# Performance work log

Hardware: AMD Instinct MI355X
Metric: run time of the kernel (lower is better)

## Reference

```python
import jax, jax.numpy as jnp
import numpy as np

D = 512      # d_model
S = 8        # num_quantum_states
B, T = 16, 1024
LN_EPS = 1e-5


def setup_inputs() -> dict:
    key = jax.random.key(0)
    ks = jax.random.split(key, 10)
    sc = lambda fan_in: 1.0 / np.sqrt(fan_in)
    return {
        "x": jax.random.normal(ks[0], (B, T, D), dtype=jnp.float32),
        # entanglement gates: torch Linear weight [out=D, in=2D], bias [D], stacked over S
        "W_ent": jax.random.uniform(ks[1], (S, D, 2 * D), minval=-sc(2 * D), maxval=sc(2 * D)),
        "b_ent": jax.random.uniform(ks[2], (S, D), minval=-sc(2 * D), maxval=sc(2 * D)),
        # measurement MLP: Linear(D*S->D), LayerNorm(D), Tanh, Linear(D->1)
        "m1_w": jax.random.uniform(ks[3], (D, D * S), minval=-sc(D * S), maxval=sc(D * S)),
        "m1_b": jax.random.uniform(ks[4], (D,), minval=-sc(D * S), maxval=sc(D * S)),
        "ln_g": jnp.ones((D,), dtype=jnp.float32),
        "ln_b": jnp.zeros((D,), dtype=jnp.float32),
        "m2_w": jax.random.uniform(ks[5], (1, D), minval=-sc(D), maxval=sc(D)),
        "m2_b": jax.random.uniform(ks[6], (1,), minval=-sc(D), maxval=sc(D)),
    }


def _layernorm(h, g, b):
    mu = jnp.mean(h, axis=-1, keepdims=True)
    var = jnp.mean(jnp.square(h - mu), axis=-1, keepdims=True)
    return (h - mu) * jax.lax.rsqrt(var + LN_EPS) * g + b


def reference(x, W_ent, b_ent, m1_w, m1_b, ln_g, ln_b, m2_w, m2_b):
    b_, t_, d_ = x.shape
    s_ = W_ent.shape[0]
    # gate(cat[x_i, x_j]).mean(dim=2) == x_i @ W1^T + mean_j(x_j) @ W2^T + b  (exact algebra)
    W1 = W_ent[:, :, :d_]   # [S, D, D] acts on x_i
    W2 = W_ent[:, :, d_:]   # [S, D, D] acts on x_j (mean over j)
    xbar = jnp.mean(x, axis=1)                                   # [B, D]
    ent = (jnp.einsum('btd,sed->bste', x, W1)                    # [B, S, T, D]
           + jnp.einsum('bd,sed->bse', xbar, W2)[:, :, None, :]
           + b_ent[None, :, None, :])
    # permute(0,2,3,1).reshape(B,T,D*S): feature layout is (d, s) fastest on s
    qv = jnp.transpose(ent, (0, 2, 3, 1)).reshape(b_, t_, d_ * s_)
    h = jnp.tanh(_layernorm(qv @ m1_w.T + m1_b, ln_g, ln_b))     # [B, T, D]
    attn_logits = h @ m2_w.T + m2_b                              # [B, T, 1]
    attn_weights = jax.nn.softmax(attn_logits, axis=1)
    context = jnp.sum(attn_weights * x, axis=1)                  # [B, D]
    return context, attn_weights
```

## Files before the change

kernel.cpp:

```cpp
#include <hip/hip_runtime.h>
#include <hip/hip_bf16.h>

typedef __attribute__((ext_vector_type(8))) short bf16x8;
typedef __attribute__((ext_vector_type(4))) float f32x4;

__device__ __forceinline__ float bf2f(unsigned short u) {
    union { unsigned int i; float f; } c; c.i = ((unsigned int)u) << 16; return c.f;
}
__device__ __forceinline__ unsigned short f2bf(float f) {
    union { float f; unsigned int i; } c; c.f = f;
    unsigned int x = c.i;
    x += 0x7fffu + ((x >> 16) & 1u);
    return (unsigned short)(x >> 16);
}
__device__ __forceinline__ unsigned int pk2(float a, float b) {
    __hip_bfloat162 h = __float22bfloat162_rn(float2{a, b});
    union { __hip_bfloat162 h; unsigned int u; } c; c.h = h; return c.u;
}
__device__ __forceinline__ float tanh_fast(float v) {
    float a = fabsf(v);
    a = fminf(a, 15.0f);
    float e = __expf(2.0f * a);
    float t = 1.0f - 2.0f / (e + 1.0f);
    return copysignf(t, v);
}

#define GLOAD_LDS16(gp, lp) \
    __builtin_amdgcn_global_load_lds((const __attribute__((address_space(1))) void*)(gp), \
                                     (__attribute__((address_space(3))) void*)(lp), 16, 0, 0)

#define MFMA(a, b, c) __builtin_amdgcn_mfma_f32_16x16x32_bf16((a), (b), (c), 0, 0, 0)

#define SBAR()  __builtin_amdgcn_s_barrier()
#define SCHED0() __builtin_amdgcn_sched_barrier(0)


__global__ void k_sumx(const float* __restrict__ x, float* __restrict__ sumx) {
    int b = blockIdx.x, tc = blockIdx.y;
    int tid = threadIdx.x;
    const float* xp = x + ((size_t)b * 1024 + tc * 64) * 512;
    float a0 = 0.f, a1 = 0.f;
    for (int t = 0; t < 64; ++t) {
        a0 += xp[(size_t)t * 512 + tid];
        a1 += xp[(size_t)t * 512 + tid + 256];
    }
    atomicAdd(&sumx[b * 512 + tid], a0);
    atomicAdd(&sumx[b * 512 + tid + 256], a1);
}

__global__ void k_prepA(const float* __restrict__ m1w, const float* __restrict__ bent,
                        unsigned short* __restrict__ Abf, float* __restrict__ bias2) {
    int i = blockIdx.x, tid = threadIdx.x;
    const float* row = m1w + (size_t)i * 4096;
    float acc = 0.f;
    #pragma unroll
    for (int q = 0; q < 4; ++q) {
        int col = q * 1024 + tid * 4;
        float4 v = *(const float4*)(row + col);
        ushort4 o;
        o.x = f2bf(v.x); o.y = f2bf(v.y); o.z = f2bf(v.z); o.w = f2bf(v.w);
        *(ushort4*)(Abf + (size_t)i * 4096 + col) = o;
        int e0 = col >> 3, s0 = col & 7;
        acc += v.x * bent[(s0    ) * 512 + e0];
        acc += v.y * bent[(s0 + 1) * 512 + e0];
        acc += v.z * bent[(s0 + 2) * 512 + e0];
        acc += v.w * bent[(s0 + 3) * 512 + e0];
    }
    #pragma unroll
    for (int off = 32; off; off >>= 1) acc += __shfl_xor(acc, off);
    __shared__ float r4[4];
    if ((tid & 63) == 0) r4[tid >> 6] = acc;
    __syncthreads();
    if (tid == 0) bias2[i] = r4[0] + r4[1] + r4[2] + r4[3];
}

__global__ void k_conv_W(const float* __restrict__ W, unsigned short* __restrict__ WT) {
    __shared__ float tile[128][33];
    int e0 = blockIdx.x * 16;
    int j0 = blockIdx.y * 32;
    int tid = threadIdx.x;
    int tx = tid & 31, ty = tid >> 5;
    #pragma unroll
    for (int q = 0; q < 16; ++q) {
        int lk = q * 8 + ty;
        int de = lk >> 3, s = lk & 7;
        int r = s * 512 + e0 + de;
        tile[lk][tx] = W[(size_t)r * 1024 + j0 + tx];
    }
    __syncthreads();
    int j = tid >> 3, ck = (tid & 7) * 16;
    unsigned short* dst = WT + (size_t)(j0 + j) * 4096 + e0 * 8 + ck;
    #pragma unroll
    for (int g = 0; g < 4; ++g) {
        ushort4 o;
        o.x = f2bf(tile[ck + g * 4 + 0][j]);
        o.y = f2bf(tile[ck + g * 4 + 1][j]);
        o.z = f2bf(tile[ck + g * 4 + 2][j]);
        o.w = f2bf(tile[ck + g * 4 + 3][j]);
        *(ushort4*)(dst + g * 4) = o;
    }
}

__launch_bounds__(512, 2)
__global__ void k_gemm1(const unsigned short* __restrict__ Abf,
                        const unsigned short* __restrict__ WT,
                        float* __restrict__ CpL, float* __restrict__ CpR) {
    __shared__ __align__(16) unsigned short sA[2][64 * 64];
    __shared__ __align__(16) unsigned short sB[2][256 * 64];
    int i0 = blockIdx.x * 64;
    int j0 = blockIdx.y * 256;
    int kbase = blockIdx.z * 512;
    int tid = threadIdx.x, lane = tid & 63, w = tid >> 6;
    int wm = w >> 2, wn = w & 3;
    int lr = lane >> 3, sl = lane & 7;
    int lo = lane & 15, hi = lane >> 4;
    int arow = w * 8 + lr;
    const unsigned short* gA = Abf + (size_t)(i0 + arow) * 4096 + kbase + ((sl ^ lr) << 3);
    const unsigned short* gB0 = WT + (size_t)(j0 + w * 32 + 0 * 8 + lr) * 4096 + kbase + ((sl ^ lr) << 3);
    const unsigned short* gB1 = WT + (size_t)(j0 + w * 32 + 1 * 8 + lr) * 4096 + kbase + ((sl ^ lr) << 3);
    const unsigned short* gB2 = WT + (size_t)(j0 + w * 32 + 2 * 8 + lr) * 4096 + kbase + ((sl ^ lr) << 3);
    const unsigned short* gB3 = WT + (size_t)(j0 + w * 32 + 3 * 8 + lr) * 4096 + kbase + ((sl ^ lr) << 3);
    bool left = (blockIdx.y < 2);
    f32x4 acc[2][4] = {};

#define G1_STAGE(tt, bufn)                                                    \
    do {                                                                      \
        int koff = (tt) * 64;                                                 \
        GLOAD_LDS16(gA + koff, &sA[bufn][w * 8 * 64]);                        \
        GLOAD_LDS16(gB0 + koff, &sB[bufn][(w * 32 + 0) * 64]);                \
        GLOAD_LDS16(gB1 + koff, &sB[bufn][(w * 32 + 8) * 64]);                \
        GLOAD_LDS16(gB2 + koff, &sB[bufn][(w * 32 + 16) * 64]);               \
        GLOAD_LDS16(gB3 + koff, &sB[bufn][(w * 32 + 24) * 64]);               \
        SCHED0();                                                             \
    } while (0)

    G1_STAGE(0, 0);
    #pragma unroll
    for (int t = 0; t < 8; ++t) {
        int buf = t & 1;
        if (t < 7) {
            G1_STAGE(t + 1, buf ^ 1);
            asm volatile("s_waitcnt vmcnt(5)" ::: "memory");
        } else {
            asm volatile("s_waitcnt vmcnt(0)" ::: "memory");
        }
        SCHED0(); SBAR(); SCHED0();
        __builtin_amdgcn_s_setprio(1);
        #pragma unroll
        for (int kk = 0; kk < 2; ++kk) {
            int slotX = ((kk * 4 + hi) ^ (lo & 7)) << 3;
            bf16x8 a0 = *(const bf16x8*)(&sA[buf][(wm * 32 +      lo) * 64 + slotX]);
            bf16x8 a1 = *(const bf16x8*)(&sA[buf][(wm * 32 + 16 + lo) * 64 + slotX]);
            #pragma unroll
            for (int n = 0; n < 4; ++n) {
                bf16x8 bb = *(const bf16x8*)(&sB[buf][(wn * 64 + n * 16 + lo) * 64 + slotX]);
                if (left) {
                    acc[0][n] = MFMA(a0, bb, acc[0][n]);
                    acc[1][n] = MFMA(a1, bb, acc[1][n]);
                } else {
                    acc[0][n] = MFMA(bb, a0, acc[0][n]);
                    acc[1][n] = MFMA(bb, a1, acc[1][n]);
                }
            }
        }
        __builtin_amdgcn_s_setprio(0);
        if (t < 7) { SCHED0(); SBAR(); SCHED0(); }
    }
#undef G1_STAGE

    int ksoff = blockIdx.z * 262144;
    if (left) {
        #pragma unroll
        for (int m = 0; m < 2; ++m) {
            int ib = i0 + wm * 32 + m * 16 + hi * 4;
            #pragma unroll
            for (int n = 0; n < 4; ++n) {
                int j = j0 + wn * 64 + n * 16 + lo;
                #pragma unroll
                for (int r = 0; r < 4; ++r)
                    CpL[ksoff + (ib + r) * 512 + j] = acc[m][n][r];
            }
        }
    } else {
        #pragma unroll
        for (int m = 0; m < 2; ++m) {
            int ic = i0 + wm * 32 + m * 16 + lo;
            #pragma unroll
            for (int n = 0; n < 4; ++n) {
                int db = j0 - 512 + wn * 64 + n * 16 + hi * 4;
                #pragma unroll
                for (int r = 0; r < 4; ++r)
                    CpR[ksoff + (db + r) * 512 + ic] = acc[m][n][r];
            }
        }
    }
}

__global__ void k_reduce(const float* __restrict__ CpL, const float* __restrict__ CpR,
                         unsigned short* __restrict__ M1bf, unsigned short* __restrict__ M2t) {
    int bx = blockIdx.x;
    const float* Cp = (bx < 256) ? CpL : CpR;
    unsigned short* ob = (bx < 256) ? M1bf : M2t;
    int gid = (bx & 255) * 256 + threadIdx.x;
    float4 s = ((const float4*)Cp)[gid];
    #pragma unroll
    for (int ks = 1; ks < 8; ++ks) {
        float4 t = ((const float4*)Cp)[ks * 65536 + gid];
        s.x += t.x; s.y += t.y; s.z += t.z; s.w += t.w;
    }
    ushort4 o;
    o.x = f2bf(s.x); o.y = f2bf(s.y); o.z = f2bf(s.z); o.w = f2bf(s.w);
    ((ushort4*)ob)[gid] = o;
}

__global__ void k_cb(const float* __restrict__ sumx, const unsigned short* __restrict__ M2t,
                     const float* __restrict__ bias2, const float* __restrict__ m1b,
                     float* __restrict__ cbo) {
    int b = blockIdx.x, i0 = blockIdx.y * 64;
    int tid = threadIdx.x;
    int il = tid & 63, dq = tid >> 6;
    const float* sx = sumx + b * 512 + dq * 128;
    const unsigned short* mp = M2t + (size_t)dq * 128 * 512 + i0 + il;
    float acc = 0.f;
    #pragma unroll 4
    for (int dd = 0; dd < 128; ++dd)
        acc += sx[dd] * bf2f(mp[(size_t)dd * 512]);
    __shared__ float sPart[4][64];
    sPart[dq][il] = acc;
    __syncthreads();
    if (tid < 64) {
        float v = sPart[0][tid] + sPart[1][tid] + sPart[2][tid] + sPart[3][tid];
        cbo[b * 512 + i0 + tid] = v * (1.0f / 1024.0f) + bias2[i0 + tid] + m1b[i0 + tid];
    }
}

__launch_bounds__(512)
__global__ void k_gemm2s(const float* __restrict__ x,
                         const unsigned short* __restrict__ M1bf,
                         unsigned short* __restrict__ ypk) {
    __shared__ __align__(16) unsigned short sA[64 * 64];
    __shared__ __align__(16) unsigned short sB[512 * 64];
    int bt0 = blockIdx.x * 64;
    int tid = threadIdx.x, lane = tid & 63, w = tid >> 6;
    int wm = w >> 2, wn = w & 3;
    int lo = lane & 15, hi = lane >> 4;
    int lr = lane >> 3, sl = lane & 7;
    int arow = tid >> 3, aslot = tid & 7;
    const float* gA = x + (size_t)(bt0 + arow) * 512 + aslot * 8;
    unsigned short* dAp = sA + arow * 64 + ((aslot ^ (arow & 7)) << 3);
    const unsigned short* gB[8];
    #pragma unroll
    for (int g = 0; g < 8; ++g)
        gB[g] = M1bf + (size_t)(w * 64 + g * 8 + lr) * 512 + ((sl ^ lr) << 3);
    f32x4 acc[2][8] = {};
    for (int k0 = 0; k0 < 512; k0 += 64) {
        if (k0) __syncthreads();
        #pragma unroll
        for (int g = 0; g < 8; ++g)
            GLOAD_LDS16(gB[g] + k0, &sB[(w * 64 + g * 8) * 64]);
        float4 f0 = *(const float4*)(gA + k0);
        float4 f1 = *(const float4*)(gA + k0 + 4);
        bf16x8 pk;
        pk[0] = (short)f2bf(f0.x); pk[1] = (short)f2bf(f0.y);
        pk[2] = (short)f2bf(f0.z); pk[3] = (short)f2bf(f0.w);
        pk[4] = (short)f2bf(f1.x); pk[5] = (short)f2bf(f1.y);
        pk[6] = (short)f2bf(f1.z); pk[7] = (short)f2bf(f1.w);
        *(bf16x8*)dAp = pk;
        __syncthreads();
        #pragma unroll
        for (int kk = 0; kk < 2; ++kk) {
            int slotX = ((kk * 4 + hi) ^ (lo & 7)) << 3;
            bf16x8 a0 = *(const bf16x8*)(sA + (wm * 32 +      lo) * 64 + slotX);
            bf16x8 a1 = *(const bf16x8*)(sA + (wm * 32 + 16 + lo) * 64 + slotX);
            #pragma unroll
            for (int n = 0; n < 8; ++n) {
                bf16x8 bb = *(const bf16x8*)(sB + (wn * 128 + n * 16 + lo) * 64 + slotX);
                acc[0][n] = MFMA(a0, bb, acc[0][n]);
                acc[1][n] = MFMA(a1, bb, acc[1][n]);
            }
        }
    }
    unsigned short* yb = ypk + (size_t)blockIdx.x * 32768;
    #pragma unroll
    for (int m = 0; m < 2; ++m) {
        #pragma unroll
        for (int n = 0; n < 8; ++n) {
            unsigned int u0 = pk2(acc[m][n][0], acc[m][n][1]);
            unsigned int u1 = pk2(acc[m][n][2], acc[m][n][3]);
            uint2 o; o.x = u0; o.y = u1;
            *(uint2*)(yb + (((w * 16 + m * 8 + n) << 8) + (lane << 2))) = o;
        }
    }
}

__launch_bounds__(512)
__global__ void k_lnlogit(const unsigned short* __restrict__ ypk,
                          const float* __restrict__ cb,
                          const float* __restrict__ lng, const float* __restrict__ lnb,
                          const float* __restrict__ m2w, const float* __restrict__ m2b,
                          float* __restrict__ logits) {
    __shared__ __align__(16) unsigned short sY[32768];
    __shared__ float sCb[512], sG[512], sBe[512], sW[512];
    __shared__ float sS1[64][8], sS2[64][8], sLg[64][8];
    int blk = blockIdx.x;
    int bt0 = blk * 64;
    int b = bt0 >> 10;
    int tid = threadIdx.x, w = tid >> 6, lane = tid & 63;
    sCb[tid] = cb[b * 512 + tid];
    sG[tid]  = lng[tid];
    sBe[tid] = lnb[tid];
    sW[tid]  = m2w[tid];
    const unsigned short* src = ypk + (size_t)blk * 32768;
    #pragma unroll
    for (int it = 0; it < 8; ++it) {
        int off = (w * 8 + it) * 512;
        GLOAD_LDS16(src + off + (lane << 3), &sY[off]);
    }
    asm volatile("s_waitcnt vmcnt(0)" ::: "memory");
    __syncthreads();

    int row = tid >> 3, sub = tid & 7;
    int wm = row >> 5, m = (row >> 4) & 1, hi = (row >> 2) & 3, r = row & 3;
    float s1 = 0.f, s2 = 0.f;
    #pragma unroll
    for (int wn = 0; wn < 4; ++wn) {
        #pragma unroll
        for (int n = 0; n < 8; ++n) {
            int c = (wm * 4 + wn) * 16 + m * 8 + n;
            int eb = c * 256 + r;
            int ib = wn * 128 + n * 16;
            #pragma unroll
            for (int l2 = 0; l2 < 2; ++l2) {
                int lo = sub * 2 + l2;
                float v = bf2f(sY[eb + (hi * 16 + lo) * 4]) + sCb[ib + lo];
                s1 += v; s2 += v * v;
            }
        }
    }
    sS1[row][sub] = s1; sS2[row][sub] = s2;
    __syncthreads();
    float a1 = 0.f, a2 = 0.f;
    #pragma unroll
    for (int q = 0; q < 8; ++q) { a1 += sS1[row][q]; a2 += sS2[row][q]; }
    float mu = a1 * (1.0f / 512.0f);
    float var = a2 * (1.0f / 512.0f) - mu * mu;
    float rs = rsqrtf(var + 1e-5f);
    float lg = 0.f;
    #pragma unroll
    for (int wn = 0; wn < 4; ++wn) {
        #pragma unroll
        for (int n = 0; n < 8; ++n) {
            int c = (wm * 4 + wn) * 16 + m * 8 + n;
            int eb = c * 256 + r;
            int ib = wn * 128 + n * 16;
            #pragma unroll
            for (int l2 = 0; l2 < 2; ++l2) {
                int lo = sub * 2 + l2;
                float v = bf2f(sY[eb + (hi * 16 + lo) * 4]) + sCb[ib + lo];
                float h = tanh_fast((v - mu) * rs * sG[ib + lo] + sBe[ib + lo]);
                lg += h * sW[ib + lo];
            }
        }
    }
    sLg[row][sub] = lg;
    __syncthreads();
    if (sub == 0) {
        float t = 0.f;
        #pragma unroll
        for (int q = 0; q < 8; ++q) t += sLg[row][q];
        logits[bt0 + row] = t + m2b[0];
    }
}

__global__ void k_softmax(const float* __restrict__ logits, float* __restrict__ wout) {
    int b = blockIdx.x, tid = threadIdx.x;
    __shared__ float red[4];
    float4 v = ((const float4*)(logits + b * 1024))[tid];
    float mx = fmaxf(fmaxf(v.x, v.y), fmaxf(v.z, v.w));
    for (int off = 32; off; off >>= 1) mx = fmaxf(mx, __shfl_xor(mx, off));
    if ((tid & 63) == 0) red[tid >> 6] = mx;
    __syncthreads();
    mx = fmaxf(fmaxf(red[0], red[1]), fmaxf(red[2], red[3]));
    float e0 = expf(v.x - mx), e1 = expf(v.y - mx), e2 = expf(v.z - mx), e3 = expf(v.w - mx);
    float sm = e0 + e1 + e2 + e3;
    for (int off = 32; off; off >>= 1) sm += __shfl_xor(sm, off);
    __syncthreads();
    if ((tid & 63) == 0) red[tid >> 6] = sm;
    __syncthreads();
    float inv = 1.0f / (red[0] + red[1] + red[2] + red[3]);
    float4 o; o.x = e0 * inv; o.y = e1 * inv; o.z = e2 * inv; o.w = e3 * inv;
    ((float4*)(wout + b * 1024))[tid] = o;
}

__global__ void k_context(const float* __restrict__ x, const float* __restrict__ wts,
                          float* __restrict__ ctx) {
    int b = blockIdx.x, tc = blockIdx.y;
    int tid = threadIdx.x;
    const float* xp = x + ((size_t)b * 1024 + tc * 64) * 512;
    const float* wp = wts + b * 1024 + tc * 64;
    float a0 = 0.f, a1 = 0.f;
    for (int t = 0; t < 64; ++t) {
        float wv = wp[t];
        a0 += wv * xp[(size_t)t * 512 + tid];
        a1 += wv * xp[(size_t)t * 512 + tid + 256];
    }
    atomicAdd(&ctx[b * 512 + tid], a0);
    atomicAdd(&ctx[b * 512 + tid + 256], a1);
}

extern "C" void kernel_launch(void* const* d_in, const int* in_sizes, int n_in,
                              void* d_out, int out_size, void* d_ws, size_t ws_size,
                              hipStream_t stream) {
    (void)in_sizes; (void)n_in; (void)out_size; (void)ws_size;
    const float* x    = (const float*)d_in[0];
    const float* Went = (const float*)d_in[1];
    const float* bent = (const float*)d_in[2];
    const float* m1w  = (const float*)d_in[3];
    const float* m1b  = (const float*)d_in[4];
    const float* lng  = (const float*)d_in[5];
    const float* lnb  = (const float*)d_in[6];
    const float* m2w  = (const float*)d_in[7];
    const float* m2b  = (const float*)d_in[8];
    float* out = (float*)d_out;
    char* ws = (char*)d_ws;

    unsigned short* Abf   = (unsigned short*)(ws);
    unsigned short* WT    = (unsigned short*)(ws + 4194304);
    float* CpL            = (float*)(ws + 12582912);
    float* CpR            = (float*)(ws + 20971520);
    unsigned short* ypk   = (unsigned short*)(ws + 12582912);
    unsigned short* M1bf  = (unsigned short*)(ws + 29360128);
    unsigned short* M2t   = (unsigned short*)(ws + 29884416);
    float* sumx   = (float*)(ws + 30408704);
    float* bias2  = (float*)(ws + 30441472);
    float* cb     = (float*)(ws + 30443520);
    float* logits = (float*)(ws + 30476288);

    hipMemsetAsync(sumx, 0, 512 * 16 * sizeof(float), stream);
    hipMemsetAsync(out, 0, 8192 * sizeof(float), stream);

    k_sumx<<<dim3(16, 16), 256, 0, stream>>>(x, sumx);
    k_prepA<<<512, 256, 0, stream>>>(m1w, bent, Abf, bias2);
    k_conv_W<<<dim3(32, 32), 256, 0, stream>>>(Went, WT);
    k_gemm1<<<dim3(8, 4, 8), 512, 0, stream>>>(Abf, WT, CpL, CpR);
    k_reduce<<<512, 256, 0, stream>>>(CpL, CpR, M1bf, M2t);
    k_cb<<<dim3(16, 8), 256, 0, stream>>>(sumx, M2t, bias2, m1b, cb);
    k_gemm2s<<<256, 512, 0, stream>>>(x, M1bf, ypk);
    k_lnlogit<<<256, 512, 0, stream>>>(ypk, cb, lng, lnb, m2w, m2b, logits);
    k_softmax<<<16, 256, 0, stream>>>(logits, out + 8192);
    k_context<<<dim3(16, 16), 256, 0, stream>>>(x, out + 8192, out);
}
```

Baseline: 98.89 us.

## Fuse LayerNorm/logit into GEMM epilogue, merge softmax with context, drop atomics

Fuses the LayerNorm, tanh and logit epilogue into the second GEMM kernel, staging its output tile in the reused shared B buffer instead of writing it to global memory and reloading it in a separate kernel. Softmax is merged into the context kernel, where each block recomputes the per-batch softmax, and per-chunk partial sums replace atomics and memsets for both the x sum and the context, with small reduce passes added. This removes two kernel launches, two memsets and a global round trip of the intermediate. In exchange softmax work is done redundantly in each block and the GEMM kernel carries extra shared memory and register pressure.

After: 86.06 us. 13.0% less time.

```diff
diff --git a/kernel.cpp b/kernel.cpp
--- a/kernel.cpp
+++ b/kernel.cpp
@@ -35,7 +35,7 @@
 #define SCHED0() __builtin_amdgcn_sched_barrier(0)
 
 
-__global__ void k_sumx(const float* __restrict__ x, float* __restrict__ sumx) {
+__global__ void k_sumxp(const float* __restrict__ x, float* __restrict__ sumxp) {
     int b = blockIdx.x, tc = blockIdx.y;
     int tid = threadIdx.x;
     const float* xp = x + ((size_t)b * 1024 + tc * 64) * 512;
@@ -44,8 +44,9 @@
         a0 += xp[(size_t)t * 512 + tid];
         a1 += xp[(size_t)t * 512 + tid + 256];
     }
-    atomicAdd(&sumx[b * 512 + tid], a0);
-    atomicAdd(&sumx[b * 512 + tid + 256], a1);
+    float* o = sumxp + (size_t)(b * 16 + tc) * 512;
+    o[tid] = a0;
+    o[tid + 256] = a1;
 }
 
 __global__ void k_prepA(const float* __restrict__ m1w, const float* __restrict__ bent,
@@ -213,18 +214,26 @@
     ((ushort4*)ob)[gid] = o;
 }
 
-__global__ void k_cb(const float* __restrict__ sumx, const unsigned short* __restrict__ M2t,
+__global__ void k_cb(const float* __restrict__ sumxp, const unsigned short* __restrict__ M2t,
                      const float* __restrict__ bias2, const float* __restrict__ m1b,
                      float* __restrict__ cbo) {
     int b = blockIdx.x, i0 = blockIdx.y * 64;
     int tid = threadIdx.x;
+    __shared__ float sSx[512];
+    for (int d = tid; d < 512; d += 256) {
+        float s = 0.f;
+        #pragma unroll
+        for (int p = 0; p < 16; ++p)
+            s += sumxp[(size_t)(b * 16 + p) * 512 + d];
+        sSx[d] = s;
+    }
+    __syncthreads();
     int il = tid & 63, dq = tid >> 6;
-    const float* sx = sumx + b * 512 + dq * 128;
     const unsigned short* mp = M2t + (size_t)dq * 128 * 512 + i0 + il;
     float acc = 0.f;
     #pragma unroll 4
     for (int dd = 0; dd < 128; ++dd)
-        acc += sx[dd] * bf2f(mp[(size_t)dd * 512]);
+        acc += sSx[dq * 128 + dd] * bf2f(mp[(size_t)dd * 512]);
     __shared__ float sPart[4][64];
     sPart[dq][il] = acc;
     __syncthreads();
@@ -235,16 +244,26 @@
 }
 
 __launch_bounds__(512)
-__global__ void k_gemm2s(const float* __restrict__ x,
+__global__ void k_gemm2f(const float* __restrict__ x,
                          const unsigned short* __restrict__ M1bf,
-                         unsigned short* __restrict__ ypk) {
+                         const float* __restrict__ cb,
+                         const float* __restrict__ lng, const float* __restrict__ lnb,
+                         const float* __restrict__ m2w, const float* __restrict__ m2b,
+                         float* __restrict__ logits) {
     __shared__ __align__(16) unsigned short sA[64 * 64];
     __shared__ __align__(16) unsigned short sB[512 * 64];
+    __shared__ float sCb[512], sG[512], sBe[512], sW[512];
+    __shared__ float sS1[64][8], sS2[64][8], sLg[64][8];
     int bt0 = blockIdx.x * 64;
+    int b = bt0 >> 10;
     int tid = threadIdx.x, lane = tid & 63, w = tid >> 6;
     int wm = w >> 2, wn = w & 3;
     int lo = lane & 15, hi = lane >> 4;
     int lr = lane >> 3, sl = lane & 7;
+    sCb[tid] = cb[b * 512 + tid];
+    sG[tid]  = lng[tid];
+    sBe[tid] = lnb[tid];
+    sW[tid]  = m2w[tid];
     int arow = tid >> 3, aslot = tid & 7;
     const float* gA = x + (size_t)(bt0 + arow) * 512 + aslot * 8;
     unsigned short* dAp = sA + arow * 64 + ((aslot ^ (arow & 7)) << 3);
@@ -280,7 +299,8 @@
             }
         }
     }
-    unsigned short* yb = ypk + (size_t)blockIdx.x * 32768;
+    __syncthreads();
+    unsigned short* sY = sB;
     #pragma unroll
     for (int m = 0; m < 2; ++m) {
         #pragma unroll
@@ -288,93 +308,69 @@
             unsigned int u0 = pk2(acc[m][n][0], acc[m][n][1]);
             unsigned int u1 = pk2(acc[m][n][2], acc[m][n][3]);
             uint2 o; o.x = u0; o.y = u1;
-            *(uint2*)(yb + (((w * 16 + m * 8 + n) << 8) + (lane << 2))) = o;
-        }
-    }
-}
-
-__launch_bounds__(512)
-__global__ void k_lnlogit(const unsigned short* __restrict__ ypk,
-                          const float* __restrict__ cb,
-                          const float* __restrict__ lng, const float* __restrict__ lnb,
-                          const float* __restrict__ m2w, const float* __restrict__ m2b,
-                          float* __restrict__ logits) {
-    __shared__ __align__(16) unsigned short sY[32768];
-    __shared__ float sCb[512], sG[512], sBe[512], sW[512];
-    __shared__ float sS1[64][8], sS2[64][8], sLg[64][8];
-    int blk = blockIdx.x;
-    int bt0 = blk * 64;
-    int b = bt0 >> 10;
-    int tid = threadIdx.x, w = tid >> 6, lane = tid & 63;
-    sCb[tid] = cb[b * 512 + tid];
-    sG[tid]  = lng[tid];
-    sBe[tid] = lnb[tid];
-    sW[tid]  = m2w[tid];
-    const unsigned short* src = ypk + (size_t)blk * 32768;
-    #pragma unroll
-    for (int it = 0; it < 8; ++it) {
-        int off = (w * 8 + it) * 512;
-        GLOAD_LDS16(src + off + (lane << 3), &sY[off]);
-    }
-    asm volatile("s_waitcnt vmcnt(0)" ::: "memory");
-    __syncthreads();
-
-    int row = tid >> 3, sub = tid & 7;
-    int wm = row >> 5, m = (row >> 4) & 1, hi = (row >> 2) & 3, r = row & 3;
+            *(uint2*)(sY + (((w * 16 + m * 8 + n) << 8) + (lane << 2))) = o;
+        }
+    }
+    __syncthreads();
+    int erow = tid >> 3, esub = tid & 7;
+    int ewm = erow >> 5, em = (erow >> 4) & 1, ehi = (erow >> 2) & 3, er = erow & 3;
     float s1 = 0.f, s2 = 0.f;
     #pragma unroll
-    for (int wn = 0; wn < 4; ++wn) {
-        #pragma unroll
-        for (int n = 0; n < 8; ++n) {
-            int c = (wm * 4 + wn) * 16 + m * 8 + n;
-            int eb = c * 256 + r;
-            int ib = wn * 128 + n * 16;
+    for (int ewn = 0; ewn < 4; ++ewn) {
+        #pragma unroll
+        for (int en = 0; en < 8; ++en) {
+            int c = (ewm * 4 + ewn) * 16 + em * 8 + en;
+            int eb = c * 256 + er;
+            int ib = ewn * 128 + en * 16;
             #pragma unroll
             for (int l2 = 0; l2 < 2; ++l2) {
-                int lo = sub * 2 + l2;
-                float v = bf2f(sY[eb + (hi * 16 + lo) * 4]) + sCb[ib + lo];
+                int elo = esub * 2 + l2;
+                float v = bf2f(sY[eb + (ehi * 16 + elo) * 4]) + sCb[ib + elo];
                 s1 += v; s2 += v * v;
             }
         }
     }
-    sS1[row][sub] = s1; sS2[row][sub] = s2;
+    sS1[erow][esub] = s1; sS2[erow][esub] = s2;
     __syncthreads();
     float a1 = 0.f, a2 = 0.f;
     #pragma unroll
-    for (int q = 0; q < 8; ++q) { a1 += sS1[row][q]; a2 += sS2[row][q]; }
+    for (int q = 0; q < 8; ++q) { a1 += sS1[erow][q]; a2 += sS2[erow][q]; }
     float mu = a1 * (1.0f / 512.0f);
     float var = a2 * (1.0f / 512.0f) - mu * mu;
     float rs = rsqrtf(var + 1e-5f);
     float lg = 0.f;
     #pragma unroll
-    for (int wn = 0; wn < 4; ++wn) {
-        #pragma unroll
-        for (int n = 0; n < 8; ++n) {
-            int c = (wm * 4 + wn) * 16 + m * 8 + n;
-            int eb = c * 256 + r;
-            int ib = wn * 128 + n * 16;
+    for (int ewn = 0; ewn < 4; ++ewn) {
+        #pragma unroll
+        for (int en = 0; en < 8; ++en) {
+            int c = (ewm * 4 + ewn) * 16 + em * 8 + en;
+            int eb = c * 256 + er;
+            int ib = ewn * 128 + en * 16;
             #pragma unroll
             for (int l2 = 0; l2 < 2; ++l2) {
-                int lo = sub * 2 + l2;
-                float v = bf2f(sY[eb + (hi * 16 + lo) * 4]) + sCb[ib + lo];
-                float h = tanh_fast((v - mu) * rs * sG[ib + lo] + sBe[ib + lo]);
-                lg += h * sW[ib + lo];
-            }
-        }
-    }
-    sLg[row][sub] = lg;
-    __syncthreads();
-    if (sub == 0) {
+                int elo = esub * 2 + l2;
+                float v = bf2f(sY[eb + (ehi * 16 + elo) * 4]) + sCb[ib + elo];
+                float h = tanh_fast((v - mu) * rs * sG[ib + elo] + sBe[ib + elo]);
+                lg += h * sW[ib + elo];
+            }
+        }
+    }
+    sLg[erow][esub] = lg;
+    __syncthreads();
+    if (esub == 0) {
         float t = 0.f;
         #pragma unroll
-        for (int q = 0; q < 8; ++q) t += sLg[row][q];
-        logits[bt0 + row] = t + m2b[0];
-    }
-}
-
-__global__ void k_softmax(const float* __restrict__ logits, float* __restrict__ wout) {
-    int b = blockIdx.x, tid = threadIdx.x;
+        for (int q = 0; q < 8; ++q) t += sLg[erow][q];
+        logits[bt0 + erow] = t + m2b[0];
+    }
+}
+
+__global__ void k_swctx(const float* __restrict__ x, const float* __restrict__ logits,
+                        float* __restrict__ ctxp, float* __restrict__ attn) {
+    int b = blockIdx.x, tc = blockIdx.y;
+    int tid = threadIdx.x;
     __shared__ float red[4];
+    __shared__ float sWt[1024];
     float4 v = ((const float4*)(logits + b * 1024))[tid];
     float mx = fmaxf(fmaxf(v.x, v.y), fmaxf(v.z, v.w));
     for (int off = 32; off; off >>= 1) mx = fmaxf(mx, __shfl_xor(mx, off));
@@ -389,23 +385,30 @@
     __syncthreads();
     float inv = 1.0f / (red[0] + red[1] + red[2] + red[3]);
     float4 o; o.x = e0 * inv; o.y = e1 * inv; o.z = e2 * inv; o.w = e3 * inv;
-    ((float4*)(wout + b * 1024))[tid] = o;
-}
-
-__global__ void k_context(const float* __restrict__ x, const float* __restrict__ wts,
-                          float* __restrict__ ctx) {
-    int b = blockIdx.x, tc = blockIdx.y;
-    int tid = threadIdx.x;
+    ((float4*)sWt)[tid] = o;
+    if (tc == 0) ((float4*)(attn + b * 1024))[tid] = o;
+    __syncthreads();
     const float* xp = x + ((size_t)b * 1024 + tc * 64) * 512;
-    const float* wp = wts + b * 1024 + tc * 64;
+    const float* wp = sWt + tc * 64;
     float a0 = 0.f, a1 = 0.f;
     for (int t = 0; t < 64; ++t) {
         float wv = wp[t];
         a0 += wv * xp[(size_t)t * 512 + tid];
         a1 += wv * xp[(size_t)t * 512 + tid + 256];
     }
-    atomicAdd(&ctx[b * 512 + tid], a0);
-    atomicAdd(&ctx[b * 512 + tid + 256], a1);
+    float* op = ctxp + (size_t)(b * 16 + tc) * 512;
+    op[tid] = a0;
+    op[tid + 256] = a1;
+}
+
+__global__ void k_ctxred(const float* __restrict__ ctxp, float* __restrict__ ctx) {
+    int idx = blockIdx.x * 256 + threadIdx.x;
+    int b = idx >> 9, d = idx & 511;
+    float s = 0.f;
+    #pragma unroll
+    for (int p = 0; p < 16; ++p)
+        s += ctxp[(size_t)(b * 16 + p) * 512 + d];
+    ctx[b * 512 + d] = s;
 }
 
 extern "C" void kernel_launch(void* const* d_in, const int* in_sizes, int n_in,
@@ -428,25 +431,21 @@
     unsigned short* WT    = (unsigned short*)(ws + 4194304);
     float* CpL            = (float*)(ws + 12582912);
     float* CpR            = (float*)(ws + 20971520);
-    unsigned short* ypk   = (unsigned short*)(ws + 12582912);
     unsigned short* M1bf  = (unsigned short*)(ws + 29360128);
     unsigned short* M2t   = (unsigned short*)(ws + 29884416);
-    float* sumx   = (float*)(ws + 30408704);
-    float* bias2  = (float*)(ws + 30441472);
-    float* cb     = (float*)(ws + 30443520);
-    float* logits = (float*)(ws + 30476288);
-
-    hipMemsetAsync(sumx, 0, 512 * 16 * sizeof(float), stream);
-    hipMemsetAsync(out, 0, 8192 * sizeof(float), stream);
-
-    k_sumx<<<dim3(16, 16), 256, 0, stream>>>(x, sumx);
+    float* sumxp  = (float*)(ws + 30408704);
+    float* ctxp   = (float*)(ws + 30932992);
+    float* bias2  = (float*)(ws + 31457280);
+    float* cb     = (float*)(ws + 31459328);
+    float* logits = (float*)(ws + 31492096);
+
+    k_sumxp<<<dim3(16, 16), 256, 0, stream>>>(x, sumxp);
     k_prepA<<<512, 256, 0, stream>>>(m1w, bent, Abf, bias2);
     k_conv_W<<<dim3(32, 32), 256, 0, stream>>>(Went, WT);
     k_gemm1<<<dim3(8, 4, 8), 512, 0, stream>>>(Abf, WT, CpL, CpR);
     k_reduce<<<512, 256, 0, stream>>>(CpL, CpR, M1bf, M2t);
-    k_cb<<<dim3(16, 8), 256, 0, stream>>>(sumx, M2t, bias2, m1b, cb);
-    k_gemm2s<<<256, 512, 0, stream>>>(x, M1bf, ypk);
-    k_lnlogit<<<256, 512, 0, stream>>>(ypk, cb, lng, lnb, m2w, m2b, logits);
-    k_softmax<<<16, 256, 0, stream>>>(logits, out + 8192);
-    k_context<<<dim3(16, 16), 256, 0, stream>>>(x, out + 8192, out);
-}
+    k_cb<<<dim3(16, 8), 256, 0, stream>>>(sumxp, M2t, bias2, m1b, cb);
+    k_gemm2f<<<256, 512, 0, stream>>>(x, M1bf, cb, lng, lnb, m2w, m2b, logits);
+    k_swctx<<<dim3(16, 16), 256, 0, stream>>>(x, logits, ctxp, out + 8192);
+    k_ctxred<<<32, 256, 0, stream>>>(ctxp, out);
+}
```
